# Kernel optimization log

Hardware: AMD Instinct MI355X
Metric: run time of the kernel (lower is better)

Reference implementation:

```python
import jax, jax.numpy as jnp
import numpy as np

T, B, DIN, H, NQ = 128, 256, 1024, 1024, 8
QDIM = H            # qdim must equal hidden_dim for f*cx elementwise product
D = DIN + H         # concat([x, hx]) feature width


def _qembed(z, enc_w, wire_w, wire_b):
    """QuantumEmbedding: linear encoder then sequential per-wire tanh updates.
    z: [B, QDIM]; enc_w: [QDIM, QDIM]; wire_w: [NQ, QDIM]; wire_b: [NQ].
    Wire i reads the CURRENT z (wires 0..i-1 already updated) -> sequential."""
    z = z @ enc_w.T
    for i in range(wire_w.shape[0]):  # small fixed loop (n_qubits)
        z = z.at[:, i].set(jnp.tanh(z @ wire_w[i] + wire_b[i]))
    return z


def setup_inputs() -> dict:
    key = jax.random.key(0)
    ks = jax.random.split(key, 14)
    s = 0.02
    return {
        "inputs": jax.random.normal(ks[0], (T, B, DIN), jnp.float32),
        # proj_to_q: Linear(D, QDIM)
        "Wq": s * jax.random.normal(ks[1], (QDIM, D), jnp.float32),
        "bq": jnp.zeros((QDIM,), jnp.float32),
        # forget quantum gate
        "enc_f": s * jax.random.normal(ks[2], (QDIM, QDIM), jnp.float32),
        "wf_w": s * jax.random.normal(ks[3], (NQ, QDIM), jnp.float32),
        "wf_b": jnp.zeros((NQ,), jnp.float32),
        # input quantum gate
        "enc_i": s * jax.random.normal(ks[4], (QDIM, QDIM), jnp.float32),
        "wi_w": s * jax.random.normal(ks[5], (NQ, QDIM), jnp.float32),
        "wi_b": jnp.zeros((NQ,), jnp.float32),
        # classical update gate: Linear(D, H)
        "Wu": s * jax.random.normal(ks[6], (H, D), jnp.float32),
        "bu": jnp.zeros((H,), jnp.float32),
        # classical output gate: Linear(D, H)
        "Wo": s * jax.random.normal(ks[7], (H, D), jnp.float32),
        "bo": jnp.zeros((H,), jnp.float32),
    }


def reference(inputs, Wq, bq, enc_f, wf_w, wf_b, enc_i, wi_w, wi_b, Wu, bu, Wo, bo):
    t, b, _ = inputs.shape
    h = Wu.shape[0]
    h0 = jnp.zeros((b, h), inputs.dtype)
    c0 = jnp.zeros((b, h), inputs.dtype)

    def step(carry, x):
        hx, cx = carry
        comb = jnp.concatenate([x, hx], axis=1)          # [B, D]
        zq = comb @ Wq.T + bq                            # [B, QDIM]
        f = jax.nn.sigmoid(_qembed(zq, enc_f, wf_w, wf_b))
        i = jax.nn.sigmoid(_qembed(zq, enc_i, wi_w, wi_b))
        g = jnp.tanh(comb @ Wu.T + bu)
        o = jax.nn.sigmoid(comb @ Wo.T + bo)
        cx = f * cx + i * g
        hx = o * jnp.tanh(cx)
        return (hx, cx), hx

    (hx, cx), outs = jax.lax.scan(step, (h0, c0), inputs)
    return outs, hx, cx
```

## Files before the change

### kernel.cpp

```cpp
#include <hip/hip_runtime.h>
#include <hip/hip_bf16.h>


#define T_STEPS 128
#define BATCH   256
#define DIN_    1024
#define HID_    1024
#define NQ_     8
#define DCAT    2048
#define NG      4096

using short8 = __attribute__((ext_vector_type(8))) short;
using f32x4  = __attribute__((ext_vector_type(4))) float;

static __device__ __forceinline__ ushort f2bf(float f) {
    union { float f; uint32_t u; } c{f};
    uint32_t u = c.u;
    uint32_t r = (u + 0x7fffu + ((u >> 16) & 1u)) >> 16;
    return (ushort)r;
}
static __device__ __forceinline__ float sigmoid_fast(float x) {
    return 1.f / (1.f + __expf(-x));
}
static __device__ __forceinline__ float tanh_fast(float x) {
    float xc = fminf(fmaxf(x, -15.f), 15.f);
    float e  = __expf(-2.f * xc);
    return (1.f - e) / (1.f + e);
}


__global__ void quant_bf16_k(const float* __restrict__ src, ushort* __restrict__ dst, int n4) {
    int i = blockIdx.x * blockDim.x + threadIdx.x;
    if (i < n4) {
        float4 v = ((const float4*)src)[i];
        ushort4 o;
        o.x = f2bf(v.x); o.y = f2bf(v.y); o.z = f2bf(v.z); o.w = f2bf(v.w);
        ((ushort4*)dst)[i] = o;
    }
}

__global__ void transpose_quant_k(const float* __restrict__ Wq, ushort* __restrict__ WqT) {
    __shared__ float tile[32][33];
    int bx = blockIdx.x;
    int by = blockIdx.y;
    int tx = threadIdx.x;
    int ty = threadIdx.y;
#pragma unroll
    for (int p = 0; p < 4; ++p)
        tile[ty + 8*p][tx] = Wq[(size_t)(by*32 + ty + 8*p) * 2048 + bx*32 + tx];
    __syncthreads();
#pragma unroll
    for (int p = 0; p < 4; ++p)
        WqT[(size_t)(bx*32 + ty + 8*p) * 1024 + by*32 + tx] = f2bf(tile[tx][ty + 8*p]);
}

__global__ void bias_merge_k(const float* __restrict__ enc, const float* __restrict__ bq,
                             float* __restrict__ out) {
    int j = blockIdx.x * blockDim.x + threadIdx.x;
    const float* row = enc + (size_t)j * 1024;
    float s = 0.f;
    for (int m = 0; m < 1024; m += 4) {
        float4 e = *(const float4*)(row + m);
        float4 b = *(const float4*)(bq + m);
        s += e.x*b.x + e.y*b.y + e.z*b.z + e.w*b.w;
    }
    out[j] = s;
}

__global__ __launch_bounds__(256) void gemm_bt_ww_k(const ushort* __restrict__ A,
                                                    const ushort* __restrict__ Bt,
                                                    ushort* __restrict__ C,
                                                    int M, int N, int K) {
    __shared__ ushort As[64][72];
    __shared__ ushort Bs[64][72];
    const int tid = threadIdx.x;
    const int tile_n = blockIdx.x * 64;
    const int tile_m = blockIdx.y * 64;
    const int r8 = tid >> 3;
    const int c8 = (tid & 7) << 3;
    const int wid = tid >> 6, lane = tid & 63;
    const int wm = (wid >> 1) * 32, wn = (wid & 1) * 32;
    const int l15 = lane & 15, lk = (lane >> 4) << 3;

    f32x4 acc00 = {0.f,0.f,0.f,0.f}, acc01 = {0.f,0.f,0.f,0.f};
    f32x4 acc10 = {0.f,0.f,0.f,0.f}, acc11 = {0.f,0.f,0.f,0.f};

    for (int k0 = 0; k0 < K; k0 += 64) {
#pragma unroll
        for (int p = 0; p < 2; ++p) {
            int row = p*32 + r8;
            *(short8*)&As[row][c8] = *(const short8*)(A  + (size_t)(tile_m + row)*K + k0 + c8);
            *(short8*)&Bs[row][c8] = *(const short8*)(Bt + (size_t)(tile_n + row)*K + k0 + c8);
        }
        __syncthreads();
#pragma unroll
        for (int ks = 0; ks < 2; ++ks) {
            short8 a0 = *(short8*)&As[wm      + l15][ks*32 + lk];
            short8 a1 = *(short8*)&As[wm + 16 + l15][ks*32 + lk];
            short8 b0 = *(short8*)&Bs[wn      + l15][ks*32 + lk];
            short8 b1 = *(short8*)&Bs[wn + 16 + l15][ks*32 + lk];
            acc00 = __builtin_amdgcn_mfma_f32_16x16x32_bf16(a0, b0, acc00, 0, 0, 0);
            acc01 = __builtin_amdgcn_mfma_f32_16x16x32_bf16(a0, b1, acc01, 0, 0, 0);
            acc10 = __builtin_amdgcn_mfma_f32_16x16x32_bf16(a1, b0, acc10, 0, 0, 0);
            acc11 = __builtin_amdgcn_mfma_f32_16x16x32_bf16(a1, b1, acc11, 0, 0, 0);
        }
        __syncthreads();
    }
    const int orow = (lane >> 4) * 4;
#pragma unroll
    for (int r = 0; r < 4; ++r) {
        int m0 = tile_m + wm + orow + r;
        int n0 = tile_n + wn + l15;
        C[(size_t)m0*N + n0]           = f2bf(acc00[r]);
        C[(size_t)m0*N + n0 + 16]      = f2bf(acc01[r]);
        C[(size_t)(m0+16)*N + n0]      = f2bf(acc10[r]);
        C[(size_t)(m0+16)*N + n0 + 16] = f2bf(acc11[r]);
    }
}

__global__ __launch_bounds__(256) void step_gemm_k(const float* __restrict__ xt,
                                                   const ushort* __restrict__ hxb,
                                                   const ushort* __restrict__ Wall,
                                                   float* __restrict__ preact) {
    __shared__ ushort As[64][72];
    __shared__ ushort Bs[64][72];
    const int tid = threadIdx.x;
    const int tile_n = blockIdx.x * 64;
    const int tile_m = blockIdx.y * 64;
    const int r8 = tid >> 3;
    const int c8 = (tid & 7) << 3;
    const int wid = tid >> 6, lane = tid & 63;
    const int wm = (wid >> 1) * 32, wn = (wid & 1) * 32;
    const int l15 = lane & 15, lk = (lane >> 4) << 3;

    f32x4 acc00 = {0.f,0.f,0.f,0.f}, acc01 = {0.f,0.f,0.f,0.f};
    f32x4 acc10 = {0.f,0.f,0.f,0.f}, acc11 = {0.f,0.f,0.f,0.f};

    for (int kt = 0; kt < DCAT/64; ++kt) {
        const int k0 = kt * 64;
        if (k0 < DIN_) {
#pragma unroll
            for (int p = 0; p < 2; ++p) {
                int row = p*32 + r8;
                const float* src = xt + (size_t)(tile_m + row)*DIN_ + k0 + c8;
                float4 v0 = *(const float4*)(src);
                float4 v1 = *(const float4*)(src + 4);
                short8 pk;
                pk[0] = (short)f2bf(v0.x); pk[1] = (short)f2bf(v0.y);
                pk[2] = (short)f2bf(v0.z); pk[3] = (short)f2bf(v0.w);
                pk[4] = (short)f2bf(v1.x); pk[5] = (short)f2bf(v1.y);
                pk[6] = (short)f2bf(v1.z); pk[7] = (short)f2bf(v1.w);
                *(short8*)&As[row][c8] = pk;
            }
        } else {
#pragma unroll
            for (int p = 0; p < 2; ++p) {
                int row = p*32 + r8;
                *(short8*)&As[row][c8] =
                    *(const short8*)(hxb + (size_t)(tile_m + row)*HID_ + (k0 - DIN_) + c8);
            }
        }
#pragma unroll
        for (int p = 0; p < 2; ++p) {
            int row = p*32 + r8;
            *(short8*)&Bs[row][c8] =
                *(const short8*)(Wall + (size_t)(tile_n + row)*DCAT + k0 + c8);
        }
        __syncthreads();
#pragma unroll
        for (int ks = 0; ks < 2; ++ks) {
            short8 a0 = *(short8*)&As[wm      + l15][ks*32 + lk];
            short8 a1 = *(short8*)&As[wm + 16 + l15][ks*32 + lk];
            short8 b0 = *(short8*)&Bs[wn      + l15][ks*32 + lk];
            short8 b1 = *(short8*)&Bs[wn + 16 + l15][ks*32 + lk];
            acc00 = __builtin_amdgcn_mfma_f32_16x16x32_bf16(a0, b0, acc00, 0, 0, 0);
            acc01 = __builtin_amdgcn_mfma_f32_16x16x32_bf16(a0, b1, acc01, 0, 0, 0);
            acc10 = __builtin_amdgcn_mfma_f32_16x16x32_bf16(a1, b0, acc10, 0, 0, 0);
            acc11 = __builtin_amdgcn_mfma_f32_16x16x32_bf16(a1, b1, acc11, 0, 0, 0);
        }
        __syncthreads();
    }
    const int orow = (lane >> 4) * 4;
#pragma unroll
    for (int r = 0; r < 4; ++r) {
        int m0 = tile_m + wm + orow + r;
        int n0 = tile_n + wn + l15;
        preact[(size_t)m0*NG + n0]           = acc00[r];
        preact[(size_t)m0*NG + n0 + 16]      = acc01[r];
        preact[(size_t)(m0+16)*NG + n0]      = acc10[r];
        preact[(size_t)(m0+16)*NG + n0 + 16] = acc11[r];
    }
}

__global__ __launch_bounds__(128) void step_pointwise_k(
        const float* __restrict__ preact,
        const float* __restrict__ wfw, const float* __restrict__ wfb,
        const float* __restrict__ wiw, const float* __restrict__ wib,
        const float* __restrict__ bu,  const float* __restrict__ bo,
        const float* __restrict__ bias_zf, const float* __restrict__ bias_zi,
        float* __restrict__ cx, ushort* __restrict__ hxb,
        float* __restrict__ dout, int t) {
    __shared__ float zrow[2][1024];
    const int b = blockIdx.x;
    const int tid = threadIdx.x;
    const int wid = tid >> 6;
    const int lane = tid & 63;

    const float* pre  = preact + (size_t)b*NG + wid*HID_;
    const float* bias = wid == 0 ? bias_zf : bias_zi;
    const float* ww   = wid == 0 ? wfw : wiw;
    const float* wb   = wid == 0 ? wfb : wib;

    float z[16];
#pragma unroll
    for (int j = 0; j < 16; ++j) z[j] = pre[j*64 + lane] + bias[j*64 + lane];

#pragma unroll
    for (int w = 0; w < NQ_; ++w) {
        float p = 0.f;
#pragma unroll
        for (int j = 0; j < 16; ++j) p += z[j] * ww[(size_t)w*1024 + j*64 + lane];
#pragma unroll
        for (int off = 1; off < 64; off <<= 1) p += __shfl_xor(p, off, 64);
        float s = tanh_fast(p + wb[w]);
        if (lane == w) z[0] = s;
    }
#pragma unroll
    for (int j = 0; j < 16; ++j) zrow[wid][j*64 + lane] = z[j];
    __syncthreads();

    const float* prow = preact + (size_t)b*NG;
#pragma unroll
    for (int e = 0; e < 8; ++e) {
        int k = e*128 + tid;
        float f  = sigmoid_fast(zrow[0][k]);
        float ig = sigmoid_fast(zrow[1][k]);
        float g  = tanh_fast(prow[2048 + k] + bu[k]);
        float o  = sigmoid_fast(prow[3072 + k] + bo[k]);
        float c  = f * cx[(size_t)b*HID_ + k] + ig * g;
        cx[(size_t)b*HID_ + k] = c;
        float h  = o * tanh_fast(c);
        dout[(size_t)t*BATCH*HID_ + (size_t)b*HID_ + k] = h;
        hxb[(size_t)b*HID_ + k] = f2bf(h);
        if (t == T_STEPS - 1) {
            dout[(size_t)T_STEPS*BATCH*HID_ + (size_t)b*HID_ + k] = h;
            dout[(size_t)T_STEPS*BATCH*HID_ + (size_t)BATCH*HID_ + (size_t)b*HID_ + k] = c;
        }
    }
}

extern "C" void kernel_launch(void* const* d_in, const int* in_sizes, int n_in,
                              void* d_out, int out_size, void* d_ws, size_t ws_size,
                              hipStream_t stream) {
    const float* inputs = (const float*)d_in[0];
    const float* Wq     = (const float*)d_in[1];
    const float* bq     = (const float*)d_in[2];
    const float* enc_f  = (const float*)d_in[3];
    const float* wf_w   = (const float*)d_in[4];
    const float* wf_b   = (const float*)d_in[5];
    const float* enc_i  = (const float*)d_in[6];
    const float* wi_w   = (const float*)d_in[7];
    const float* wi_b   = (const float*)d_in[8];
    const float* Wu     = (const float*)d_in[9];
    const float* bu     = (const float*)d_in[10];
    const float* Wo     = (const float*)d_in[11];
    const float* bo     = (const float*)d_in[12];
    float* out = (float*)d_out;

    char* ws = (char*)d_ws;
    ushort* Wall    = (ushort*)(ws);
    ushort* WqT     = (ushort*)(ws + (16u<<20));
    ushort* encfb   = (ushort*)(ws + (20u<<20));
    ushort* encib   = (ushort*)(ws + (22u<<20));
    float*  preact  = (float*) (ws + (24u<<20));
    float*  cx      = (float*) (ws + (28u<<20));
    ushort* hxb     = (ushort*)(ws + (29u<<20));
    float*  bias_zf = (float*) (ws + (30u<<20));
    float*  bias_zi = (float*) (ws + (30u<<20) + 4096);

    hipMemsetAsync(cx,  0, (size_t)BATCH*HID_*sizeof(float), stream);
    hipMemsetAsync(hxb, 0, (size_t)BATCH*HID_*sizeof(ushort), stream);

    quant_bf16_k<<<(1024*1024/4 + 255)/256, 256, 0, stream>>>(enc_f, encfb, 1024*1024/4);
    quant_bf16_k<<<(1024*1024/4 + 255)/256, 256, 0, stream>>>(enc_i, encib, 1024*1024/4);
    quant_bf16_k<<<(1024*2048/4 + 255)/256, 256, 0, stream>>>(Wu, Wall + (size_t)2048*2048, 1024*2048/4);
    quant_bf16_k<<<(1024*2048/4 + 255)/256, 256, 0, stream>>>(Wo, Wall + (size_t)3072*2048, 1024*2048/4);
    transpose_quant_k<<<dim3(64, 32), dim3(32, 8), 0, stream>>>(Wq, WqT);
    bias_merge_k<<<4, 256, 0, stream>>>(enc_f, bq, bias_zf);
    bias_merge_k<<<4, 256, 0, stream>>>(enc_i, bq, bias_zi);

    gemm_bt_ww_k<<<dim3(2048/64, 1024/64), 256, 0, stream>>>(encfb, WqT, Wall, 1024, 2048, 1024);
    gemm_bt_ww_k<<<dim3(2048/64, 1024/64), 256, 0, stream>>>(encib, WqT, Wall + (size_t)1024*2048, 1024, 2048, 1024);

    for (int t = 0; t < T_STEPS; ++t) {
        step_gemm_k<<<dim3(NG/64, BATCH/64), 256, 0, stream>>>(
            inputs + (size_t)t*BATCH*DIN_, hxb, Wall, preact);
        step_pointwise_k<<<256, 128, 0, stream>>>(
            preact, wf_w, wf_b, wi_w, wi_b, bu, bo, bias_zf, bias_zi,
            cx, hxb, out, t);
    }
}
```

Measured before the change: 5.995 ms.

## Split-K step GEMM with async LDS double buffering and pre-quantized inputs

Converts all time-step inputs to bf16 once up front instead of converting inside every step GEMM. The per-step GEMM is split along K (input half and hidden half) into two partial outputs, which doubles the grid to fill more CUs. Operand tiles are loaded with global_load_lds into a double-buffered, XOR-swizzled LDS layout so the next tile's loads overlap the MFMAs. The pointwise kernel sums the two partials and spreads the gate activations across four waves. In exchange it adds an extra partial-output buffer to write and read each step, plus a large bf16 copy of the inputs.

```diff
diff --git a/kernel.cpp b/kernel.cpp
--- a/kernel.cpp
+++ b/kernel.cpp
@@ -1,5 +1,6 @@
 #include <hip/hip_runtime.h>
 #include <hip/hip_bf16.h>
+#include <stdint.h>
 
 
 #define T_STEPS 128
@@ -27,6 +28,11 @@
     float e  = __expf(-2.f * xc);
     return (1.f - e) / (1.f + e);
 }
+static __device__ __forceinline__ void gload_lds16(const ushort* g, ushort* l) {
+    __builtin_amdgcn_global_load_lds(
+        (const __attribute__((address_space(1))) void*)g,
+        (__attribute__((address_space(3))) void*)l, 16, 0, 0);
+}
 
 
 __global__ void quant_bf16_k(const float* __restrict__ src, ushort* __restrict__ dst, int n4) {
@@ -41,10 +47,8 @@
 
 __global__ void transpose_quant_k(const float* __restrict__ Wq, ushort* __restrict__ WqT) {
     __shared__ float tile[32][33];
-    int bx = blockIdx.x;
-    int by = blockIdx.y;
-    int tx = threadIdx.x;
-    int ty = threadIdx.y;
+    int bx = blockIdx.x, by = blockIdx.y;
+    int tx = threadIdx.x, ty = threadIdx.y;
 #pragma unroll
     for (int p = 0; p < 4; ++p)
         tile[ty + 8*p][tx] = Wq[(size_t)(by*32 + ty + 8*p) * 2048 + bx*32 + tx];
@@ -82,8 +86,7 @@
     const int wm = (wid >> 1) * 32, wn = (wid & 1) * 32;
     const int l15 = lane & 15, lk = (lane >> 4) << 3;
 
-    f32x4 acc00 = {0.f,0.f,0.f,0.f}, acc01 = {0.f,0.f,0.f,0.f};
-    f32x4 acc10 = {0.f,0.f,0.f,0.f}, acc11 = {0.f,0.f,0.f,0.f};
+    f32x4 acc00 = {0,0,0,0}, acc01 = {0,0,0,0}, acc10 = {0,0,0,0}, acc11 = {0,0,0,0};
 
     for (int k0 = 0; k0 < K; k0 += 64) {
 #pragma unroll
@@ -118,133 +121,169 @@
     }
 }
 
-__global__ __launch_bounds__(256) void step_gemm_k(const float* __restrict__ xt,
-                                                   const ushort* __restrict__ hxb,
-                                                   const ushort* __restrict__ Wall,
-                                                   float* __restrict__ preact) {
-    __shared__ ushort As[64][72];
-    __shared__ ushort Bs[64][72];
+__global__ __launch_bounds__(256, 2) void step_gemm2_k(
+        const ushort* __restrict__ xbf, const ushort* __restrict__ hxb,
+        const ushort* __restrict__ Wall,
+        float* __restrict__ pre0, float* __restrict__ pre1, int t) {
+    __shared__ ushort smem[2][8192];
+
     const int tid = threadIdx.x;
+    const int wv = tid >> 6, ln = tid & 63;
+    const int l15 = ln & 15, hk = ln >> 4;
     const int tile_n = blockIdx.x * 64;
     const int tile_m = blockIdx.y * 64;
-    const int r8 = tid >> 3;
-    const int c8 = (tid & 7) << 3;
-    const int wid = tid >> 6, lane = tid & 63;
-    const int wm = (wid >> 1) * 32, wn = (wid & 1) * 32;
-    const int l15 = lane & 15, lk = (lane >> 4) << 3;
-
-    f32x4 acc00 = {0.f,0.f,0.f,0.f}, acc01 = {0.f,0.f,0.f,0.f};
-    f32x4 acc10 = {0.f,0.f,0.f,0.f}, acc11 = {0.f,0.f,0.f,0.f};
-
-    for (int kt = 0; kt < DCAT/64; ++kt) {
-        const int k0 = kt * 64;
-        if (k0 < DIN_) {
-#pragma unroll
-            for (int p = 0; p < 2; ++p) {
-                int row = p*32 + r8;
-                const float* src = xt + (size_t)(tile_m + row)*DIN_ + k0 + c8;
-                float4 v0 = *(const float4*)(src);
-                float4 v1 = *(const float4*)(src + 4);
-                short8 pk;
-                pk[0] = (short)f2bf(v0.x); pk[1] = (short)f2bf(v0.y);
-                pk[2] = (short)f2bf(v0.z); pk[3] = (short)f2bf(v0.w);
-                pk[4] = (short)f2bf(v1.x); pk[5] = (short)f2bf(v1.y);
-                pk[6] = (short)f2bf(v1.z); pk[7] = (short)f2bf(v1.w);
-                *(short8*)&As[row][c8] = pk;
+    const int kh = blockIdx.z;
+
+    const ushort* Asrc = kh ? (hxb + (size_t)tile_m * 1024)
+                            : (xbf + ((size_t)t * BATCH + tile_m) * 1024);
+    const ushort* Bsrc = Wall + (size_t)tile_n * DCAT + kh * 1024;
+    float* pre = kh ? pre1 : pre0;
+
+    const int wm = (wv >> 1) * 32, wn = (wv & 1) * 32;
+
+    f32x4 acc[2][2] = {{{0,0,0,0},{0,0,0,0}},{{0,0,0,0},{0,0,0,0}}};
+
+    const int srow = ln >> 3;
+    const int scol = (ln & 7) * 8;
+    const int scs  = scol ^ (srow << 3);
+
+#define STAGE(BUFI, IT)                                                          \
+    do {                                                                         \
+        const int kof_ = (IT) * 64;                                              \
+        _Pragma("unroll")                                                        \
+        for (int j = 0; j < 4; ++j) {                                            \
+            const int c_ = j * 4 + wv;                                           \
+            const int r_ = (c_ & 7) * 8 + srow;                                  \
+            const ushort* src_ = (c_ < 8)                                        \
+                ? Asrc + (size_t)r_ * 1024 + kof_ + scs                          \
+                : Bsrc + (size_t)r_ * 2048 + kof_ + scs;                         \
+            gload_lds16(src_, &smem[BUFI][c_ * 512]);                            \
+        }                                                                        \
+    } while (0)
+
+    STAGE(0, 0);
+    asm volatile("s_waitcnt vmcnt(0)" ::: "memory");
+    __builtin_amdgcn_s_barrier();
+
+    int cur = 0;
+#pragma unroll 1
+    for (int it = 0; it < 16; ++it) {
+        if (it + 1 < 16) STAGE(cur ^ 1, it + 1);
+
+        const ushort* buf = smem[cur];
+        short8 a[2][2], b[2][2];
+#pragma unroll
+        for (int ks = 0; ks < 2; ++ks) {
+            const int kc = ks * 32 + hk * 8;
+#pragma unroll
+            for (int mi = 0; mi < 2; ++mi) {
+                const int r = wm + mi * 16 + l15;
+                a[mi][ks] = *(const short8*)&buf[r * 64 + (kc ^ ((r & 7) << 3))];
             }
-        } else {
-#pragma unroll
-            for (int p = 0; p < 2; ++p) {
-                int row = p*32 + r8;
-                *(short8*)&As[row][c8] =
-                    *(const short8*)(hxb + (size_t)(tile_m + row)*HID_ + (k0 - DIN_) + c8);
+#pragma unroll
+            for (int ni = 0; ni < 2; ++ni) {
+                const int r = wn + ni * 16 + l15;
+                b[ni][ks] = *(const short8*)&buf[4096 + r * 64 + (kc ^ ((r & 7) << 3))];
             }
         }
 #pragma unroll
-        for (int p = 0; p < 2; ++p) {
-            int row = p*32 + r8;
-            *(short8*)&Bs[row][c8] =
-                *(const short8*)(Wall + (size_t)(tile_n + row)*DCAT + k0 + c8);
-        }
-        __syncthreads();
-#pragma unroll
-        for (int ks = 0; ks < 2; ++ks) {
-            short8 a0 = *(short8*)&As[wm      + l15][ks*32 + lk];
-            short8 a1 = *(short8*)&As[wm + 16 + l15][ks*32 + lk];
-            short8 b0 = *(short8*)&Bs[wn      + l15][ks*32 + lk];
-            short8 b1 = *(short8*)&Bs[wn + 16 + l15][ks*32 + lk];
-            acc00 = __builtin_amdgcn_mfma_f32_16x16x32_bf16(a0, b0, acc00, 0, 0, 0);
-            acc01 = __builtin_amdgcn_mfma_f32_16x16x32_bf16(a0, b1, acc01, 0, 0, 0);
-            acc10 = __builtin_amdgcn_mfma_f32_16x16x32_bf16(a1, b0, acc10, 0, 0, 0);
-            acc11 = __builtin_amdgcn_mfma_f32_16x16x32_bf16(a1, b1, acc11, 0, 0, 0);
-        }
-        __syncthreads();
-    }
-    const int orow = (lane >> 4) * 4;
-#pragma unroll
-    for (int r = 0; r < 4; ++r) {
-        int m0 = tile_m + wm + orow + r;
-        int n0 = tile_n + wn + l15;
-        preact[(size_t)m0*NG + n0]           = acc00[r];
-        preact[(size_t)m0*NG + n0 + 16]      = acc01[r];
-        preact[(size_t)(m0+16)*NG + n0]      = acc10[r];
-        preact[(size_t)(m0+16)*NG + n0 + 16] = acc11[r];
-    }
-}
-
-__global__ __launch_bounds__(128) void step_pointwise_k(
-        const float* __restrict__ preact,
+        for (int ks = 0; ks < 2; ++ks)
+#pragma unroll
+            for (int mi = 0; mi < 2; ++mi)
+#pragma unroll
+                for (int ni = 0; ni < 2; ++ni)
+                    acc[mi][ni] = __builtin_amdgcn_mfma_f32_16x16x32_bf16(
+                        a[mi][ks], b[ni][ks], acc[mi][ni], 0, 0, 0);
+
+        asm volatile("s_waitcnt vmcnt(0)" ::: "memory");
+        __builtin_amdgcn_s_barrier();
+        cur ^= 1;
+    }
+#undef STAGE
+
+    const int orow = hk * 4;
+#pragma unroll
+    for (int mi = 0; mi < 2; ++mi)
+#pragma unroll
+        for (int ni = 0; ni < 2; ++ni)
+#pragma unroll
+            for (int r = 0; r < 4; ++r) {
+                int m = tile_m + wm + mi * 16 + orow + r;
+                int n = tile_n + wn + ni * 16 + l15;
+                pre[(size_t)m * NG + n] = acc[mi][ni][r];
+            }
+}
+
+__global__ __launch_bounds__(256) void step_pointwise2_k(
+        const float* __restrict__ pre0, const float* __restrict__ pre1,
         const float* __restrict__ wfw, const float* __restrict__ wfb,
         const float* __restrict__ wiw, const float* __restrict__ wib,
         const float* __restrict__ bu,  const float* __restrict__ bo,
         const float* __restrict__ bias_zf, const float* __restrict__ bias_zi,
         float* __restrict__ cx, ushort* __restrict__ hxb,
         float* __restrict__ dout, int t) {
-    __shared__ float zrow[2][1024];
+    __shared__ float zbuf[2][1024];
+    __shared__ float gbuf[1024];
+    __shared__ float obuf[1024];
     const int b = blockIdx.x;
     const int tid = threadIdx.x;
-    const int wid = tid >> 6;
-    const int lane = tid & 63;
-
-    const float* pre  = preact + (size_t)b*NG + wid*HID_;
-    const float* bias = wid == 0 ? bias_zf : bias_zi;
-    const float* ww   = wid == 0 ? wfw : wiw;
-    const float* wb   = wid == 0 ? wfb : wib;
-
-    float z[16];
-#pragma unroll
-    for (int j = 0; j < 16; ++j) z[j] = pre[j*64 + lane] + bias[j*64 + lane];
-
-#pragma unroll
-    for (int w = 0; w < NQ_; ++w) {
-        float p = 0.f;
-#pragma unroll
-        for (int j = 0; j < 16; ++j) p += z[j] * ww[(size_t)w*1024 + j*64 + lane];
-#pragma unroll
-        for (int off = 1; off < 64; off <<= 1) p += __shfl_xor(p, off, 64);
-        float s = tanh_fast(p + wb[w]);
-        if (lane == w) z[0] = s;
-    }
-#pragma unroll
-    for (int j = 0; j < 16; ++j) zrow[wid][j*64 + lane] = z[j];
+    const int wv = tid >> 6, ln = tid & 63;
+
+    const float* p0 = pre0 + (size_t)b * NG;
+    const float* p1 = pre1 + (size_t)b * NG;
+
+    if (wv < 2) {
+        const float* bias = wv ? bias_zi : bias_zf;
+        const float* ww   = wv ? wiw : wfw;
+        const float* wb   = wv ? wib : wfb;
+        const int off = wv * 1024;
+        float z[16];
+#pragma unroll
+        for (int j = 0; j < 16; ++j) {
+            int k = j * 64 + ln;
+            z[j] = p0[off + k] + p1[off + k] + bias[k];
+        }
+#pragma unroll
+        for (int w = 0; w < NQ_; ++w) {
+            float p = 0.f;
+#pragma unroll
+            for (int j = 0; j < 16; ++j) p += z[j] * ww[(size_t)w * 1024 + j * 64 + ln];
+#pragma unroll
+            for (int o = 1; o < 64; o <<= 1) p += __shfl_xor(p, o, 64);
+            float s = tanh_fast(p + wb[w]);
+            if (ln == w) z[0] = s;
+        }
+#pragma unroll
+        for (int j = 0; j < 16; ++j) zbuf[wv][j * 64 + ln] = z[j];
+    } else if (wv == 2) {
+#pragma unroll
+        for (int j = 0; j < 16; ++j) {
+            int k = j * 64 + ln;
+            gbuf[k] = tanh_fast(p0[2048 + k] + p1[2048 + k] + bu[k]);
+        }
+    } else {
+#pragma unroll
+        for (int j = 0; j < 16; ++j) {
+            int k = j * 64 + ln;
+            obuf[k] = sigmoid_fast(p0[3072 + k] + p1[3072 + k] + bo[k]);
+        }
+    }
     __syncthreads();
 
-    const float* prow = preact + (size_t)b*NG;
-#pragma unroll
-    for (int e = 0; e < 8; ++e) {
-        int k = e*128 + tid;
-        float f  = sigmoid_fast(zrow[0][k]);
-        float ig = sigmoid_fast(zrow[1][k]);
-        float g  = tanh_fast(prow[2048 + k] + bu[k]);
-        float o  = sigmoid_fast(prow[3072 + k] + bo[k]);
-        float c  = f * cx[(size_t)b*HID_ + k] + ig * g;
-        cx[(size_t)b*HID_ + k] = c;
-        float h  = o * tanh_fast(c);
-        dout[(size_t)t*BATCH*HID_ + (size_t)b*HID_ + k] = h;
-        hxb[(size_t)b*HID_ + k] = f2bf(h);
+    float* cxr = cx + (size_t)b * HID_;
+#pragma unroll
+    for (int e = 0; e < 4; ++e) {
+        int k = e * 256 + tid;
+        float f = sigmoid_fast(zbuf[0][k]);
+        float i = sigmoid_fast(zbuf[1][k]);
+        float c = f * cxr[k] + i * gbuf[k];
+        cxr[k] = c;
+        float h = obuf[k] * tanh_fast(c);
+        dout[(size_t)t * BATCH * HID_ + (size_t)b * HID_ + k] = h;
+        hxb[(size_t)b * HID_ + k] = f2bf(h);
         if (t == T_STEPS - 1) {
-            dout[(size_t)T_STEPS*BATCH*HID_ + (size_t)b*HID_ + k] = h;
-            dout[(size_t)T_STEPS*BATCH*HID_ + (size_t)BATCH*HID_ + (size_t)b*HID_ + k] = c;
+            dout[(size_t)T_STEPS * BATCH * HID_ + (size_t)b * HID_ + k] = h;
+            dout[(size_t)T_STEPS * BATCH * HID_ + (size_t)BATCH * HID_ + (size_t)b * HID_ + k] = c;
         }
     }
 }
@@ -269,34 +308,36 @@
 
     char* ws = (char*)d_ws;
     ushort* Wall    = (ushort*)(ws);
-    ushort* WqT     = (ushort*)(ws + (16u<<20));
-    ushort* encfb   = (ushort*)(ws + (20u<<20));
-    ushort* encib   = (ushort*)(ws + (22u<<20));
-    float*  preact  = (float*) (ws + (24u<<20));
-    float*  cx      = (float*) (ws + (28u<<20));
-    ushort* hxb     = (ushort*)(ws + (29u<<20));
-    float*  bias_zf = (float*) (ws + (30u<<20));
-    float*  bias_zi = (float*) (ws + (30u<<20) + 4096);
+    ushort* xbf     = (ushort*)(ws + (16u<<20));
+    float*  pre0    = (float*) (ws + (80u<<20));
+    float*  pre1    = (float*) (ws + (84u<<20));
+    float*  cx      = (float*) (ws + (88u<<20));
+    ushort* hxb     = (ushort*)(ws + (89u<<20));
+    float*  bias_zf = (float*) (ws + (89u<<20) + (512u<<10));
+    float*  bias_zi = (float*) (ws + (89u<<20) + (512u<<10) + 4096);
+    ushort* WqT     = (ushort*)(ws + (80u<<20));
+    ushort* encfb   = (ushort*)(ws + (84u<<20));
+    ushort* encib   = (ushort*)(ws + (86u<<20));
 
     hipMemsetAsync(cx,  0, (size_t)BATCH*HID_*sizeof(float), stream);
     hipMemsetAsync(hxb, 0, (size_t)BATCH*HID_*sizeof(ushort), stream);
 
-    quant_bf16_k<<<(1024*1024/4 + 255)/256, 256, 0, stream>>>(enc_f, encfb, 1024*1024/4);
-    quant_bf16_k<<<(1024*1024/4 + 255)/256, 256, 0, stream>>>(enc_i, encib, 1024*1024/4);
-    quant_bf16_k<<<(1024*2048/4 + 255)/256, 256, 0, stream>>>(Wu, Wall + (size_t)2048*2048, 1024*2048/4);
-    quant_bf16_k<<<(1024*2048/4 + 255)/256, 256, 0, stream>>>(Wo, Wall + (size_t)3072*2048, 1024*2048/4);
+    quant_bf16_k<<<1024, 256, 0, stream>>>(enc_f, encfb, 1024*1024/4);
+    quant_bf16_k<<<1024, 256, 0, stream>>>(enc_i, encib, 1024*1024/4);
+    quant_bf16_k<<<2048, 256, 0, stream>>>(Wu, Wall + (size_t)2048*DCAT, 1024*2048/4);
+    quant_bf16_k<<<2048, 256, 0, stream>>>(Wo, Wall + (size_t)3072*DCAT, 1024*2048/4);
     transpose_quant_k<<<dim3(64, 32), dim3(32, 8), 0, stream>>>(Wq, WqT);
     bias_merge_k<<<4, 256, 0, stream>>>(enc_f, bq, bias_zf);
     bias_merge_k<<<4, 256, 0, stream>>>(enc_i, bq, bias_zi);
-
-    gemm_bt_ww_k<<<dim3(2048/64, 1024/64), 256, 0, stream>>>(encfb, WqT, Wall, 1024, 2048, 1024);
-    gemm_bt_ww_k<<<dim3(2048/64, 1024/64), 256, 0, stream>>>(encib, WqT, Wall + (size_t)1024*2048, 1024, 2048, 1024);
+    gemm_bt_ww_k<<<dim3(32, 16), 256, 0, stream>>>(encfb, WqT, Wall, 1024, 2048, 1024);
+    gemm_bt_ww_k<<<dim3(32, 16), 256, 0, stream>>>(encib, WqT, Wall + (size_t)1024*DCAT, 1024, 2048, 1024);
+
+    quant_bf16_k<<<32768, 256, 0, stream>>>(inputs, xbf, T_STEPS*BATCH*DIN_/4);
 
     for (int t = 0; t < T_STEPS; ++t) {
-        step_gemm_k<<<dim3(NG/64, BATCH/64), 256, 0, stream>>>(
-            inputs + (size_t)t*BATCH*DIN_, hxb, Wall, preact);
-        step_pointwise_k<<<256, 128, 0, stream>>>(
-            preact, wf_w, wf_b, wi_w, wi_b, bu, bo, bias_zf, bias_zi,
+        step_gemm2_k<<<dim3(64, 4, 2), 256, 0, stream>>>(xbf, hxb, Wall, pre0, pre1, t);
+        step_pointwise2_k<<<256, 256, 0, stream>>>(
+            pre0, pre1, wf_w, wf_b, wi_w, wi_b, bu, bo, bias_zf, bias_zi,
             cx, hxb, out, t);
     }
 }
```

Result: slower. 6.733 ms (+12.3%).
